# Kernel optimization log

Measured on AMD Instinct MI355X. Metric: run time of the kernel, lower is better.

Reference implementation:

```python
import jax, jax.numpy as jnp
import numpy as np

B, S_IMG, S_TXT, H, D = 1, 2048, 512, 24, 128
HID = H * D  # 3072
S_TOT = S_TXT + S_IMG
IP_SCALE = 1.0
EPS = 1e-5


def setup_inputs() -> dict:
    key = jax.random.key(0)
    ks = jax.random.split(key, 16)
    r = lambda k, s: jax.random.normal(k, s, dtype=jnp.float32)
    w = lambda k, s: r(k, s) * 0.02
    theta = r(ks[15], (S_TOT, D))  # rotary angles over joint sequence
    z = lambda: jnp.zeros((HID,), jnp.float32)
    return dict(
        hidden_states=r(ks[0], (B, S_IMG, HID)),
        encoder_hidden_states=r(ks[1], (B, S_TXT, HID)),
        image_emb=r(ks[2], (B, 4, HID)),
        rope_cos=jnp.cos(theta), rope_sin=jnp.sin(theta),
        Wq=w(ks[3], (HID, HID)), bq=z(),
        Wk=w(ks[4], (HID, HID)), bk=z(),
        Wv=w(ks[5], (HID, HID)), bv=z(),
        Waq=w(ks[6], (HID, HID)), baq=z(),
        Wak=w(ks[7], (HID, HID)), bak=z(),
        Wav=w(ks[8], (HID, HID)), bav=z(),
        Wk_ip=w(ks[9], (HID, HID)),
        Wv_ip=w(ks[10], (HID, HID)),
        Wo=w(ks[11], (HID, HID)), bo=z(),
        Wao=w(ks[12], (HID, HID)), bao=z(),
    )


def _heads(x):  # [B,S,HID] -> [B,H,S,D]
    return x.reshape(x.shape[0], x.shape[1], H, D).transpose(0, 2, 1, 3)


def _unheads(x):  # [B,H,S,D] -> [B,S,HID]
    return x.transpose(0, 2, 1, 3).reshape(x.shape[0], x.shape[2], HID)


def _rmsnorm(x):  # over last dim, no affine (RMSNorm(128, affine=False))
    return x * jax.lax.rsqrt(jnp.mean(x * x, axis=-1, keepdims=True) + EPS)


def _rope(x, cos, sin):  # diffusers apply_rotary_emb, use_real, interleaved pairs
    xp = x.reshape(*x.shape[:-1], D // 2, 2)
    rot = jnp.stack([-xp[..., 1], xp[..., 0]], axis=-1).reshape(x.shape)
    return x * cos + rot * sin  # cos/sin [S,D] broadcast over [B,H,S,D]


def _sdpa(q, k, v):
    s = jnp.einsum('bhqd,bhkd->bhqk', q, k) / jnp.sqrt(jnp.asarray(D, q.dtype))
    return jnp.einsum('bhqk,bhkd->bhqd', jax.nn.softmax(s, axis=-1), v)


def _forward(hidden_states, encoder_hidden_states, image_emb, rope_cos, rope_sin,
             Wq, bq, Wk, bk, Wv, bv, Waq, baq, Wak, bak, Wav, bav,
             Wk_ip, Wv_ip, Wo, bo, Wao, bao):
    # main QKV over image-latent tokens
    q = _rmsnorm(_heads(hidden_states @ Wq.T + bq))
    k = _rmsnorm(_heads(hidden_states @ Wk.T + bk))
    v = _heads(hidden_states @ Wv.T + bv)
    # IP-adapter cross attention (query = latent q, kv from image_emb)
    k_ip = _rmsnorm(_heads(image_emb @ Wk_ip.T))
    v_ip = _heads(image_emb @ Wv_ip.T)
    ip_out = _unheads(_sdpa(q, k_ip, v_ip))  # [B,S_IMG,HID]
    # encoder (text) QKV, concat text-first as in Flux
    eq = _rmsnorm(_heads(encoder_hidden_states @ Waq.T + baq))
    ek = _rmsnorm(_heads(encoder_hidden_states @ Wak.T + bak))
    ev = _heads(encoder_hidden_states @ Wav.T + bav)
    q = jnp.concatenate([eq, q], axis=2)
    k = jnp.concatenate([ek, k], axis=2)
    v = jnp.concatenate([ev, v], axis=2)
    q = _rope(q, rope_cos, rope_sin)
    k = _rope(k, rope_cos, rope_sin)
    out = _unheads(_sdpa(q, k, v))  # [B,S_TOT,HID]
    enc_out, hid_out = out[:, :S_TXT], out[:, S_TXT:]
    hid_out = hid_out + IP_SCALE * ip_out
    hid_out = hid_out @ Wo.T + bo   # to_out[0] (+ identity dropout)
    enc_out = enc_out @ Wao.T + bao  # to_add_out
    return hid_out, enc_out


def reference(hidden_states, encoder_hidden_states, image_emb, rope_cos, rope_sin,
              Wq, bq, Wk, bk, Wv, bv, Waq, baq, Wak, bak, Wav, bav,
              Wk_ip, Wv_ip, Wo, bo, Wao, bao):
    return _forward(hidden_states, encoder_hidden_states, image_emb, rope_cos, rope_sin,
                    Wq, bq, Wk, bk, Wv, bv, Waq, baq, Wak, bak, Wav, bav,
                    Wk_ip, Wv_ip, Wo, bo, Wao, bao)
```

## Files before the change

### kernel.cpp

```cpp
#include <hip/hip_runtime.h>

typedef __bf16 bf16;
typedef __bf16 bf16x2 __attribute__((ext_vector_type(2)));
typedef __bf16 bf16x4 __attribute__((ext_vector_type(4)));
typedef __bf16 bf16x8 __attribute__((ext_vector_type(8)));
typedef float  f32x4  __attribute__((ext_vector_type(4)));

#define H_    24
#define D_    128
#define HID_  3072
#define SIMG_ 2048
#define STXT_ 512
#define STOT_ 2560
#define EPS_  1e-5f
#define SCALE_ 0.08838834764831845f
#define HH_   ((size_t)HID_*HID_)

typedef __attribute__((address_space(3))) unsigned int lds_uint;
typedef const __attribute__((address_space(1))) unsigned int glb_uint;
__device__ __forceinline__ void gll16(const void* g, void* l){
  __builtin_amdgcn_global_load_lds((glb_uint*)g, (lds_uint*)l, 16, 0, 0);
}

__device__ inline bf16x8 frag8f(const float* __restrict__ p){
  const f32x4 a = *(const f32x4*)p;
  const f32x4 b = *(const f32x4*)(p + 4);
  bf16x8 r;
  r[0]=(bf16)a[0]; r[1]=(bf16)a[1]; r[2]=(bf16)a[2]; r[3]=(bf16)a[3];
  r[4]=(bf16)b[0]; r[5]=(bf16)b[1]; r[6]=(bf16)b[2]; r[7]=(bf16)b[3];
  return r;
}

__global__ __launch_bounds__(256) void k_f2b(const float* __restrict__ src,
                                             bf16* __restrict__ dst, int n)
{
  const int i = ((int)blockIdx.x*256 + (int)threadIdx.x)*8;
  if (i + 7 < n){
    const f32x4 a = *(const f32x4*)(src + i);
    const f32x4 b = *(const f32x4*)(src + i + 4);
    bf16x8 o;
    o[0]=(bf16)a[0]; o[1]=(bf16)a[1]; o[2]=(bf16)a[2]; o[3]=(bf16)a[3];
    o[4]=(bf16)b[0]; o[5]=(bf16)b[1]; o[6]=(bf16)b[2]; o[7]=(bf16)b[3];
    *(bf16x8*)(dst + i) = o;
  }
}

__global__ __launch_bounds__(256) void k_f2bw8(
    const float* __restrict__ W0, const float* __restrict__ W1,
    const float* __restrict__ W2, const float* __restrict__ W3,
    const float* __restrict__ W4, const float* __restrict__ W5,
    const float* __restrict__ W6, const float* __restrict__ W7,
    bf16* __restrict__ out)
{
  const int wi = (int)blockIdx.y;
  const float* s = (wi==0)?W0:(wi==1)?W1:(wi==2)?W2:(wi==3)?W3:(wi==4)?W4:(wi==5)?W5:(wi==6)?W6:W7;
  bf16* d = out + (size_t)wi*HH_;
  const int i = ((int)blockIdx.x*256 + (int)threadIdx.x)*8;
  const f32x4 a = *(const f32x4*)(s + i);
  const f32x4 b = *(const f32x4*)(s + i + 4);
  bf16x8 o;
  o[0]=(bf16)a[0]; o[1]=(bf16)a[1]; o[2]=(bf16)a[2]; o[3]=(bf16)a[3];
  o[4]=(bf16)b[0]; o[5]=(bf16)b[1]; o[6]=(bf16)b[2]; o[7]=(bf16)b[3];
  *(bf16x8*)(d + i) = o;
}

#define MFMA_ __builtin_amdgcn_mfma_f32_16x16x32_bf16
#define MM(bfr, n) \
    acc[0][n]=MFMA_(af0,bfr,acc[0][n],0,0,0); acc[1][n]=MFMA_(af1,bfr,acc[1][n],0,0,0); \
    acc[2][n]=MFMA_(af2,bfr,acc[2][n],0,0,0); acc[3][n]=MFMA_(af3,bfr,acc[3][n],0,0,0);
#define WAIT6 asm volatile("s_waitcnt vmcnt(6)" ::: "memory")
#define WAIT0 asm volatile("s_waitcnt vmcnt(0)" ::: "memory")
#define NOWAIT (void)0

__device__ __forceinline__ void gemm8_core(
    const bf16* __restrict__ A, const bf16* __restrict__ W,
    int mb, int nb,
    f32x4 (&acc)[4][4],
    bf16 (&Al)[3][128][64],
    bf16 (&Bl)[3][256][64])
{
  const int t = (int)threadIdx.x;
  const int w = t >> 6, l = t & 63;
  const int lr = l & 15, lg = l >> 4;
  const int wr = w >> 2, wc = w & 3;
  const int srow = t >> 3;
  const int soff = ((t & 7) ^ (srow & 7)) * 8;

  const bf16* Abase = A + (size_t)(mb + srow)*HID_ + soff;
  const bf16* Wbase = W + (size_t)(nb + srow)*HID_ + soff;

#define SA(buf, tt, i) gll16(Abase + (size_t)(i)*64*HID_ + (tt)*64, &Al[buf][0][0] + (i)*4096 + t*8)
#define SB(buf, tt, i) gll16(Wbase + (size_t)(i)*64*HID_ + (tt)*64, &Bl[buf][0][0] + (i)*4096 + t*8)

  const int arow_ = wr*64 + lr;
  const int brow_ = wc*64 + lr;
  const int sx = lr & 7;

  SA(0,0,0); SA(0,0,1); SB(0,0,0); SB(0,0,1); SB(0,0,2); SB(0,0,3);
  SA(1,1,0); SA(1,1,1); SB(1,1,0); SB(1,1,1); SB(1,1,2); SB(1,1,3);
  WAIT6;
  __builtin_amdgcn_s_barrier();

#define TILE(C, NXT, TT, PRE, TW)                                            \
  {                                                                          \
    bf16x8 af0,af1,af2,af3,b0,b1;                                            \
    const int s0_ = (lg^sx)*8, s1_ = ((4+lg)^sx)*8;                          \
                                                        \
    af0=*(const bf16x8*)&Al[C][arow_   ][s0_];                               \
    af1=*(const bf16x8*)&Al[C][arow_+16][s0_];                               \
    af2=*(const bf16x8*)&Al[C][arow_+32][s0_];                               \
    af3=*(const bf16x8*)&Al[C][arow_+48][s0_];                               \
    b0 =*(const bf16x8*)&Bl[C][brow_   ][s0_];                               \
    b1 =*(const bf16x8*)&Bl[C][brow_+16][s0_];                               \
    if (PRE){ SA(NXT,(TT)+2,0); SA(NXT,(TT)+2,1); }                          \
    __builtin_amdgcn_s_setprio(1); MM(b0,0) MM(b1,1)                         \
    __builtin_amdgcn_s_setprio(0);                                           \
    __builtin_amdgcn_s_barrier();                                            \
                                                        \
    b0 =*(const bf16x8*)&Bl[C][brow_+32][s0_];                               \
    b1 =*(const bf16x8*)&Bl[C][brow_+48][s0_];                               \
    if (PRE){ SB(NXT,(TT)+2,0); SB(NXT,(TT)+2,1); }                          \
    __builtin_amdgcn_s_setprio(1); MM(b0,2) MM(b1,3)                         \
    __builtin_amdgcn_s_setprio(0);                                           \
    __builtin_amdgcn_s_barrier();                                            \
                                                        \
    af0=*(const bf16x8*)&Al[C][arow_   ][s1_];                               \
    af1=*(const bf16x8*)&Al[C][arow_+16][s1_];                               \
    af2=*(const bf16x8*)&Al[C][arow_+32][s1_];                               \
    af3=*(const bf16x8*)&Al[C][arow_+48][s1_];                               \
    b0 =*(const bf16x8*)&Bl[C][brow_   ][s1_];                               \
    b1 =*(const bf16x8*)&Bl[C][brow_+16][s1_];                               \
    if (PRE){ SB(NXT,(TT)+2,2); SB(NXT,(TT)+2,3); }                          \
    __builtin_amdgcn_s_setprio(1); MM(b0,0) MM(b1,1)                         \
    __builtin_amdgcn_s_setprio(0);                                           \
    __builtin_amdgcn_s_barrier();                                            \
                                                        \
    b0 =*(const bf16x8*)&Bl[C][brow_+32][s1_];                               \
    b1 =*(const bf16x8*)&Bl[C][brow_+48][s1_];                               \
    __builtin_amdgcn_s_setprio(1); MM(b0,2) MM(b1,3)                         \
    __builtin_amdgcn_s_setprio(0);                                           \
    TW;                                                                      \
    __builtin_amdgcn_s_barrier();                                            \
  }

  for (int base = 0; base < 45; base += 3){
    TILE(0, 2, base,   true, WAIT6);
    TILE(1, 0, base+1, true, WAIT6);
    TILE(2, 1, base+2, true, WAIT6);
  }
  TILE(0, 2, 45, true,  WAIT6);
  TILE(1, 0, 46, false, WAIT0);
  TILE(2, 1, 47, false, NOWAIT);
#undef TILE
#undef SA
#undef SB
}

__global__ __launch_bounds__(512, 1) void k_gemm8_qkv(
    const bf16* __restrict__ Ahid, const bf16* __restrict__ Aenc,
    const bf16* __restrict__ Wb,
    const float* bq, const float* bk, const float* bv,
    const float* baq, const float* bak, const float* bav,
    bf16* Cq, bf16* Ck, bf16* Cv, bf16* Ceq, bf16* Cek, bf16* Cev)
{
  __shared__ __align__(16) bf16 Al[3][128][64];
  __shared__ __align__(16) bf16 Bl[3][256][64];
  const int by = (int)blockIdx.y;
  const int enc = (by >= 16) ? 1 : 0;
  const int which = (int)blockIdx.x % 3;
  const int nb = ((int)blockIdx.x / 3)*256;
  const int mb = (enc ? (by - 16) : by)*128;
  const bf16* A = enc ? Aenc : Ahid;
  const int widx = which + enc*3;
  const bf16* W = Wb + (size_t)widx*HH_;
  const float* bias = (which==0) ? (enc?baq:bq) : (which==1) ? (enc?bak:bk) : (enc?bav:bv);
  bf16* Cm = (which==0) ? (enc?Ceq:Cq) : (which==1) ? (enc?Cek:Ck) : (enc?Cev:Cv);

  f32x4 acc[4][4] = {};
  gemm8_core(A, W, mb, nb, acc, Al, Bl);

  const int w = (int)(threadIdx.x >> 6), l = (int)(threadIdx.x & 63u);
  const int lr = l & 15, lg = l >> 4;
  const int wr = w >> 2, wc = w & 3;
  #pragma unroll
  for (int nf = 0; nf < 4; nf++){
    const int col = nb + wc*64 + nf*16 + lr;
    const float bvl = bias[col];
    #pragma unroll
    for (int m = 0; m < 4; m++){
      #pragma unroll
      for (int r = 0; r < 4; r++){
        const int row = mb + wr*64 + m*16 + lg*4 + r;
        Cm[(size_t)row*HID_ + col] = (bf16)(acc[m][nf][r] + bvl);
      }
    }
  }
}

__global__ __launch_bounds__(512, 1) void k_gemm8_out(
    const bf16* __restrict__ Ahid, const bf16* __restrict__ Aenc,
    const bf16* __restrict__ Wb,
    const float* bo, const float* bao, float* __restrict__ outp)
{
  __shared__ __align__(16) bf16 Al[3][128][64];
  __shared__ __align__(16) bf16 Bl[3][256][64];
  const int by = (int)blockIdx.y;
  const int enc = (by >= 16) ? 1 : 0;
  const int nb = (int)blockIdx.x*256;
  const int mb = (enc ? (by - 16) : by)*128;
  const bf16* A = enc ? Aenc : Ahid;
  const bf16* W = Wb + (size_t)(enc ? 7 : 6)*HH_;
  const float* bias = enc ? bao : bo;
  float* C = outp + (enc ? (size_t)SIMG_*HID_ : 0);

  f32x4 acc[4][4] = {};
  gemm8_core(A, W, mb, nb, acc, Al, Bl);

  const int w = (int)(threadIdx.x >> 6), l = (int)(threadIdx.x & 63u);
  const int lr = l & 15, lg = l >> 4;
  const int wr = w >> 2, wc = w & 3;
  #pragma unroll
  for (int nf = 0; nf < 4; nf++){
    const int col = nb + wc*64 + nf*16 + lr;
    const float bvl = bias[col];
    #pragma unroll
    for (int m = 0; m < 4; m++){
      #pragma unroll
      for (int r = 0; r < 4; r++){
        const int row = mb + wr*64 + m*16 + lg*4 + r;
        C[(size_t)row*HID_ + col] = acc[m][nf][r] + bvl;
      }
    }
  }
}

__global__ __launch_bounds__(256) void k_gemm_ip(const float* __restrict__ A,
    const float* __restrict__ Wk_, const float* __restrict__ Wv_,
    bf16* __restrict__ Ck_, bf16* __restrict__ Cv_)
{
  const float* Wm = blockIdx.y ? Wv_ : Wk_;
  bf16* C = blockIdx.y ? Cv_ : Ck_;
  const int w = (int)(threadIdx.x >> 6), l = (int)(threadIdx.x & 63u);
  const int lr = l & 15, lg = l >> 4;
  const int nbw = (int)blockIdx.x*64 + w*16;
  f32x4 acc = {};
  const float* arow = A + (size_t)((lr < 4) ? lr : 0)*HID_;
  const float* wrow = Wm + (size_t)(nbw + lr)*HID_;
  for (int k0 = 0; k0 < HID_; k0 += 32){
    const bf16x8 af  = frag8f(arow + k0 + lg*8);
    const bf16x8 bfr = frag8f(wrow + k0 + lg*8);
    acc = __builtin_amdgcn_mfma_f32_16x16x32_bf16(af, bfr, acc, 0, 0, 0);
  }
  if (lg == 0){
    #pragma unroll
    for (int r = 0; r < 4; r++)
      C[(size_t)r*HID_ + nbw + lr] = (bf16)acc[r];
  }
}

__global__ __launch_bounds__(256) void k_finish_qk(
    const bf16* __restrict__ rawQ, const bf16* __restrict__ rawK,
    const bf16* __restrict__ rawEQ, const bf16* __restrict__ rawEK,
    const float* __restrict__ cosT, const float* __restrict__ sinT,
    bf16* __restrict__ Qh, bf16* __restrict__ Kh)
{
  const int wid = (int)blockIdx.x*4 + (int)(threadIdx.x >> 6);
  const int l = (int)(threadIdx.x & 63u);
  const int s = wid / H_;
  const int h = wid % H_;
  const bf16 *sq_, *sk_;
  if (s < STXT_){
    const size_t off = (size_t)s*HID_ + h*D_;
    sq_ = rawEQ + off; sk_ = rawEK + off;
  } else {
    const size_t off = (size_t)(s - STXT_)*HID_ + h*D_;
    sq_ = rawQ + off; sk_ = rawK + off;
  }
  const int d0 = 2*l, d1 = 2*l + 1;
  float q0 = sq_[d0], q1 = sq_[d1];
  float k0 = sk_[d0], k1 = sk_[d1];
  float ssq = q0*q0 + q1*q1;
  float ssk = k0*k0 + k1*k1;
  #pragma unroll
  for (int m = 1; m < 64; m <<= 1){ ssq += __shfl_xor(ssq, m); ssk += __shfl_xor(ssk, m); }
  const float rq = rsqrtf(ssq*(1.0f/128.0f) + EPS_);
  const float rk = rsqrtf(ssk*(1.0f/128.0f) + EPS_);
  q0 *= rq; q1 *= rq; k0 *= rk; k1 *= rk;
  const float c0 = cosT[(size_t)s*D_ + d0], c1 = cosT[(size_t)s*D_ + d1];
  const float s0 = sinT[(size_t)s*D_ + d0], s1 = sinT[(size_t)s*D_ + d1];
  const float qo0 = q0*c0 - q1*s0, qo1 = q1*c1 + q0*s1;
  const float ko0 = k0*c0 - k1*s0, ko1 = k1*c1 + k0*s1;
  const size_t qoff = ((size_t)h*STOT_ + s)*D_ + d0;
  Qh[qoff] = (bf16)qo0; Qh[qoff + 1] = (bf16)qo1;
  Kh[qoff] = (bf16)ko0; Kh[qoff + 1] = (bf16)ko1;
}

__global__ __launch_bounds__(256) void k_vtrans(
    const bf16* __restrict__ rawV, const bf16* __restrict__ rawEV,
    bf16* __restrict__ Vt)
{
  __shared__ bf16 lt[128*130];
  const int t = (int)threadIdx.x;
  const int stile = (int)blockIdx.x*128;
  const int h = (int)blockIdx.y;
  #pragma unroll
  for (int i = 0; i < 8; i++){
    const int sl = i*16 + (t >> 4);
    const int s = stile + sl;
    const bf16* src = (s < STXT_) ? (rawEV + (size_t)s*HID_) : (rawV + (size_t)(s - STXT_)*HID_);
    const bf16x8 v = *(const bf16x8*)(src + h*D_ + (t & 15)*8);
    #pragma unroll
    for (int j = 0; j < 8; j++) lt[((t & 15)*8 + j)*130 + sl] = v[j];
  }
  __syncthreads();
  #pragma unroll
  for (int j = 0; j < 4; j++){
    const int d = j*32 + (t >> 3);
    const int s0 = (t & 7)*16;
    bf16x8 a, b;
    #pragma unroll
    for (int k = 0; k < 4; k++){
      const bf16x2 p = *(const bf16x2*)(lt + d*130 + s0 + 2*k);
      a[2*k] = p[0]; a[2*k+1] = p[1];
    }
    #pragma unroll
    for (int k = 0; k < 4; k++){
      const bf16x2 p = *(const bf16x2*)(lt + d*130 + s0 + 8 + 2*k);
      b[2*k] = p[0]; b[2*k+1] = p[1];
    }
    bf16* dst = Vt + ((size_t)h*D_ + d)*STOT_ + stile + s0;
    *(bf16x8*)dst = a;
    *(bf16x8*)(dst + 8) = b;
  }
}

__global__ __launch_bounds__(256) void k_finish_ip(
    const bf16* __restrict__ rawKip, const bf16* __restrict__ rawVip,
    float* __restrict__ Kip, float* __restrict__ Vip)
{
  const int wid = (int)blockIdx.x*4 + (int)(threadIdx.x >> 6);
  const int l = (int)(threadIdx.x & 63u);
  const int h = wid / 4, j = wid % 4;
  const int d0 = 2*l, d1 = 2*l + 1;
  const size_t src = (size_t)j*HID_ + h*D_;
  float k0 = rawKip[src + d0], k1 = rawKip[src + d1];
  float v0 = rawVip[src + d0], v1 = rawVip[src + d1];
  float ss = k0*k0 + k1*k1;
  #pragma unroll
  for (int m = 1; m < 64; m <<= 1) ss += __shfl_xor(ss, m);
  const float rk = rsqrtf(ss*(1.0f/128.0f) + EPS_);
  const size_t dst = ((size_t)h*4 + j)*D_;
  Kip[dst + d0] = k0*rk; Kip[dst + d1] = k1*rk;
  Vip[dst + d0] = v0;    Vip[dst + d1] = v1;
}

__global__ __launch_bounds__(256) void k_ip_attn(
    const bf16* __restrict__ rawQ, const float* __restrict__ Kip,
    const float* __restrict__ Vip, bf16* __restrict__ ipOut)
{
  const int wid = (int)blockIdx.x*4 + (int)(threadIdx.x >> 6);
  const int l = (int)(threadIdx.x & 63u);
  const int s = wid / H_, h = wid % H_;
  const int d0 = 2*l, d1 = 2*l + 1;
  const bf16* src = rawQ + (size_t)s*HID_ + h*D_;
  float q0 = src[d0], q1 = src[d1];
  float ss = q0*q0 + q1*q1;
  #pragma unroll
  for (int m = 1; m < 64; m <<= 1) ss += __shfl_xor(ss, m);
  const float r = rsqrtf(ss*(1.0f/128.0f) + EPS_);
  q0 *= r; q1 *= r;
  const float* kb = Kip + (size_t)h*4*D_;
  const float* vb = Vip + (size_t)h*4*D_;
  float sc[4];
  #pragma unroll
  for (int j = 0; j < 4; j++) sc[j] = q0*kb[j*D_ + d0] + q1*kb[j*D_ + d1];
  #pragma unroll
  for (int m = 1; m < 64; m <<= 1){
    #pragma unroll
    for (int j = 0; j < 4; j++) sc[j] += __shfl_xor(sc[j], m);
  }
  const float mx = fmaxf(fmaxf(sc[0], sc[1]), fmaxf(sc[2], sc[3]));
  float p[4], ps = 0.f;
  #pragma unroll
  for (int j = 0; j < 4; j++){ p[j] = __expf((sc[j] - mx)*SCALE_); ps += p[j]; }
  const float inv = 1.0f/ps;
  float o0 = 0.f, o1 = 0.f;
  #pragma unroll
  for (int j = 0; j < 4; j++){ o0 += p[j]*vb[j*D_ + d0]; o1 += p[j]*vb[j*D_ + d1]; }
  const size_t dst = (size_t)s*HID_ + h*D_;
  ipOut[dst + d0] = (bf16)(o0*inv);
  ipOut[dst + d1] = (bf16)(o1*inv);
}

__global__ __launch_bounds__(256, 2) void k_flash3(
    const bf16* __restrict__ Q, const bf16* __restrict__ K,
    const bf16* __restrict__ Vt, bf16* __restrict__ attnOut)
{
  __shared__ __align__(16) bf16 Ks[2][64*128];
  __shared__ __align__(16) bf16 Vs[2][128*64];
  __shared__ __align__(16) bf16 plds[4][32*64];
  const int t = (int)threadIdx.x;
  const int w = t >> 6, l = t & 63;
  const int lr = l & 15, lg = l >> 4;
  const int h = (int)blockIdx.x / 20;
  const int qbase = ((int)blockIdx.x % 20)*128 + w*32;
  const bf16* Qh = Q  + (size_t)h*STOT_*D_;
  const bf16* Kh = K  + (size_t)h*STOT_*D_;
  const bf16* Vh = Vt + (size_t)h*D_*STOT_;

  bf16x8 qf[2][4];
  #pragma unroll
  for (int qt = 0; qt < 2; qt++)
    #pragma unroll
    for (int kk = 0; kk < 4; kk++)
      qf[qt][kk] = *(const bf16x8*)(Qh + (size_t)(qbase + qt*16 + lr)*D_ + kk*32 + lg*8);

  f32x4 acc[2][8] = {};
  float mrun[2] = {-3.0e38f, -3.0e38f}, lrun[2] = {0.f, 0.f};

  const int krow = t >> 4, kslot = t & 15;
  const int vrow = t >> 3, vslot = t & 7;

  auto STAGE = [&](int buf, int kv){
    #pragma unroll
    for (int i = 0; i < 4; i++){
      const int r = i*16 + krow;
      gll16(Kh + (size_t)(kv + r)*D_ + ((kslot ^ (r & 7))*8),
            (void*)(&Ks[buf][0] + (size_t)t*8 + i*2048));
    }
    #pragma unroll
    for (int i = 0; i < 4; i++){
      const int r = i*32 + vrow;
      gll16(Vh + (size_t)r*STOT_ + kv + ((vslot ^ (r & 7))*8),
            (void*)(&Vs[buf][0] + (size_t)t*8 + i*2048));
    }
  };

  STAGE(0, 0);
  __syncthreads();
  int cur = 0;
  for (int kv = 0; kv < STOT_; kv += 64){
    if (kv + 64 < STOT_) STAGE(cur ^ 1, kv + 64);

    f32x4 st[2][4] = {};
    #pragma unroll
    for (int tt = 0; tt < 4; tt++){
      const int kr = tt*16 + lr;
      #pragma unroll
      for (int kk = 0; kk < 4; kk++){
        const bf16x8 kf = *(const bf16x8*)(&Ks[cur][0] + kr*128 + (((kk*4 + lg) ^ (kr & 7))*8));
        st[0][tt] = __builtin_amdgcn_mfma_f32_16x16x32_bf16(kf, qf[0][kk], st[0][tt], 0, 0, 0);
        st[1][tt] = __builtin_amdgcn_mfma_f32_16x16x32_bf16(kf, qf[1][kk], st[1][tt], 0, 0, 0);
      }
    }
    #pragma unroll
    for (int qt = 0; qt < 2; qt++){
      const int q = qt*16 + lr;
      float sv[4][4];
      float vmax = -3.0e38f;
      #pragma unroll
      for (int tt = 0; tt < 4; tt++)
        #pragma unroll
        for (int r = 0; r < 4; r++){ const float x = st[qt][tt][r]*SCALE_; sv[tt][r] = x; vmax = fmaxf(vmax, x); }
      vmax = fmaxf(vmax, __shfl_xor(vmax, 16));
      vmax = fmaxf(vmax, __shfl_xor(vmax, 32));
      const float mnew  = fmaxf(mrun[qt], vmax);
      const float alpha = __expf(mrun[qt] - mnew);
      float rs = 0.f;
      #pragma unroll
      for (int tt = 0; tt < 4; tt++){
        bf16x4 pq;
        #pragma unroll
        for (int r = 0; r < 4; r++){
          const float p = __expf(sv[tt][r] - mnew);
          rs += p;
          pq[r] = (bf16)p;
        }
        *(bf16x4*)(&plds[w][q*64 + (((tt*2 + (lg >> 1)) ^ (q & 7))*8) + (lg & 1)*4]) = pq;
      }
      rs += __shfl_xor(rs, 16);
      rs += __shfl_xor(rs, 32);
      lrun[qt] = lrun[qt]*alpha + rs;
      mrun[qt] = mnew;
      #pragma unroll
      for (int n = 0; n < 8; n++)
        #pragma unroll
        for (int r = 0; r < 4; r++) acc[qt][n][r] *= alpha;
    }
    #pragma unroll
    for (int ks = 0; ks < 2; ks++){
      const bf16x8 pb0 = *(const bf16x8*)(&plds[w][(lr)*64      + (((ks*4 + lg) ^ (lr & 7))*8)]);
      const bf16x8 pb1 = *(const bf16x8*)(&plds[w][(16 + lr)*64 + (((ks*4 + lg) ^ (lr & 7))*8)]);
      #pragma unroll
      for (int n = 0; n < 8; n++){
        const int vr = n*16 + lr;
        const bf16x8 vf = *(const bf16x8*)(&Vs[cur][0] + vr*64 + (((ks*4 + lg) ^ (vr & 7))*8));
        acc[0][n] = __builtin_amdgcn_mfma_f32_16x16x32_bf16(vf, pb0, acc[0][n], 0, 0, 0);
        acc[1][n] = __builtin_amdgcn_mfma_f32_16x16x32_bf16(vf, pb1, acc[1][n], 0, 0, 0);
      }
    }
    __syncthreads();
    cur ^= 1;
  }
  #pragma unroll
  for (int qt = 0; qt < 2; qt++){
    const float inv = 1.0f/lrun[qt];
    #pragma unroll
    for (int n = 0; n < 8; n++){
      #pragma unroll
      for (int r = 0; r < 4; r++){
        attnOut[(size_t)(qbase + qt*16 + lr)*HID_ + h*D_ + n*16 + lg*4 + r] = (bf16)(acc[qt][n][r]*inv);
      }
    }
  }
}

__global__ __launch_bounds__(256) void k_add_hid(
    const bf16* __restrict__ attn, const bf16* __restrict__ ip, bf16* __restrict__ outp)
{
  const size_t i = ((size_t)blockIdx.x*256 + threadIdx.x)*4;
  const bf16x4 a = *(const bf16x4*)(attn + (size_t)STXT_*HID_ + i);
  const bf16x4 b = *(const bf16x4*)(ip + i);
  bf16x4 o;
  #pragma unroll
  for (int c = 0; c < 4; c++) o[c] = (bf16)((float)a[c] + (float)b[c]);
  *(bf16x4*)(outp + i) = o;
}

extern "C" void kernel_launch(void* const* d_in, const int* in_sizes, int n_in,
                              void* d_out, int out_size, void* d_ws, size_t ws_size,
                              hipStream_t stream)
{
  const float* HS   = (const float*)d_in[0];
  const float* ENC  = (const float*)d_in[1];
  const float* IMG  = (const float*)d_in[2];
  const float* COS  = (const float*)d_in[3];
  const float* SIN  = (const float*)d_in[4];
  const float* Wq   = (const float*)d_in[5];  const float* bq  = (const float*)d_in[6];
  const float* Wk   = (const float*)d_in[7];  const float* bk  = (const float*)d_in[8];
  const float* Wv   = (const float*)d_in[9];  const float* bv  = (const float*)d_in[10];
  const float* Waq  = (const float*)d_in[11]; const float* baq = (const float*)d_in[12];
  const float* Wak  = (const float*)d_in[13]; const float* bak = (const float*)d_in[14];
  const float* Wav  = (const float*)d_in[15]; const float* bav = (const float*)d_in[16];
  const float* Wkip = (const float*)d_in[17]; const float* Wvip= (const float*)d_in[18];
  const float* Wo   = (const float*)d_in[19]; const float* bo  = (const float*)d_in[20];
  const float* Wao  = (const float*)d_in[21]; const float* bao = (const float*)d_in[22];

  char* wsb = (char*)d_ws;
  size_t off = 0;
  auto alloc = [&](size_t bytes) -> char* {
    char* p = wsb + off; off += (bytes + 255) & ~((size_t)255); return p;
  };
  bf16* rawQ   = (bf16*)alloc((size_t)SIMG_*HID_*2);
  bf16* rawK   = (bf16*)alloc((size_t)SIMG_*HID_*2);
  bf16* rawV   = (bf16*)alloc((size_t)SIMG_*HID_*2);
  bf16* rawEQ  = (bf16*)alloc((size_t)STXT_*HID_*2);
  bf16* rawEK  = (bf16*)alloc((size_t)STXT_*HID_*2);
  bf16* rawEV  = (bf16*)alloc((size_t)STXT_*HID_*2);
  bf16* rawKip = (bf16*)alloc((size_t)4*HID_*2);
  bf16* rawVip = (bf16*)alloc((size_t)4*HID_*2);
  bf16* Qb     = (bf16*)alloc((size_t)H_*STOT_*D_*2);
  bf16* Kb     = (bf16*)alloc((size_t)H_*STOT_*D_*2);
  bf16* Vtb    = (bf16*)alloc((size_t)H_*STOT_*D_*2);
  bf16* AOUT   = (bf16*)alloc((size_t)STOT_*HID_*2);
  bf16* IPOUT  = (bf16*)alloc((size_t)SIMG_*HID_*2);
  float* KIPF  = (float*)alloc((size_t)H_*4*D_*4);
  float* VIPF  = (float*)alloc((size_t)H_*4*D_*4);
  bf16* HSb    = (bf16*)alloc((size_t)SIMG_*HID_*2);
  bf16* ENCb   = (bf16*)alloc((size_t)STXT_*HID_*2);
  bf16* Wb8    = (bf16*)alloc((size_t)8*HH_*2);
  bf16* HIDIN  = HSb;

  dim3 blk(256);
  dim3 blk512(512);
  k_f2b<<<dim3(3072), blk, 0, stream>>>(HS,  HSb,  SIMG_*HID_);
  k_f2b<<<dim3(768),  blk, 0, stream>>>(ENC, ENCb, STXT_*HID_);
  k_f2bw8<<<dim3(4608,8), blk, 0, stream>>>(Wq, Wk, Wv, Waq, Wak, Wav, Wo, Wao, Wb8);
  k_gemm8_qkv<<<dim3(36,20), blk512, 0, stream>>>(HSb, ENCb, Wb8,
                                                  bq, bk, bv, baq, bak, bav,
                                                  rawQ, rawK, rawV, rawEQ, rawEK, rawEV);
  k_gemm_ip<<<dim3(48,2), blk, 0, stream>>>(IMG, Wkip, Wvip, rawKip, rawVip);
  k_finish_qk<<<dim3(15360), blk, 0, stream>>>(rawQ, rawK, rawEQ, rawEK, COS, SIN, Qb, Kb);
  k_vtrans<<<dim3(20,24), blk, 0, stream>>>(rawV, rawEV, Vtb);
  k_finish_ip<<<dim3(24), blk, 0, stream>>>(rawKip, rawVip, KIPF, VIPF);
  k_ip_attn<<<dim3(12288), blk, 0, stream>>>(rawQ, KIPF, VIPF, IPOUT);
  k_flash3<<<dim3(480), blk, 0, stream>>>(Qb, Kb, Vtb, AOUT);
  k_add_hid<<<dim3(6144), blk, 0, stream>>>(AOUT, IPOUT, HIDIN);
  float* outp = (float*)d_out;
  k_gemm8_out<<<dim3(12,20), blk512, 0, stream>>>(HIDIN, AOUT, Wb8, bo, bao, outp);
}
```

Measured before the change: 568.1 us.

## Fuse prep and finish kernels, remap blocks per XCD, drop GEMM barriers

Merges the fp32-to-bf16 conversions and the IP-adapter projection into one prep kernel. It also merges the QK finish, V transpose and IP finish into one kernel, and folds the IP-output add into the flash-attention epilogue using vectorized bf16x4 stores, which removes the separate add kernel and its global round-trip. The GEMM and flash grids become 1-D with a remap that groups neighbouring tiles per XCD for better L2 reuse. Three intra-tile barriers are removed from the GEMM main loop to cut synchronisation stalls. The risk is a possible LDS race if the prefetch into the next buffer overlaps reads that other waves have not finished.

Measured after the change: 612.0 us. 1.08x slower.

```diff
diff --git a/kernel.cpp b/kernel.cpp
--- a/kernel.cpp
+++ b/kernel.cpp
@@ -31,31 +31,7 @@
   return r;
 }
 
-__global__ __launch_bounds__(256) void k_f2b(const float* __restrict__ src,
-                                             bf16* __restrict__ dst, int n)
-{
-  const int i = ((int)blockIdx.x*256 + (int)threadIdx.x)*8;
-  if (i + 7 < n){
-    const f32x4 a = *(const f32x4*)(src + i);
-    const f32x4 b = *(const f32x4*)(src + i + 4);
-    bf16x8 o;
-    o[0]=(bf16)a[0]; o[1]=(bf16)a[1]; o[2]=(bf16)a[2]; o[3]=(bf16)a[3];
-    o[4]=(bf16)b[0]; o[5]=(bf16)b[1]; o[6]=(bf16)b[2]; o[7]=(bf16)b[3];
-    *(bf16x8*)(dst + i) = o;
-  }
-}
-
-__global__ __launch_bounds__(256) void k_f2bw8(
-    const float* __restrict__ W0, const float* __restrict__ W1,
-    const float* __restrict__ W2, const float* __restrict__ W3,
-    const float* __restrict__ W4, const float* __restrict__ W5,
-    const float* __restrict__ W6, const float* __restrict__ W7,
-    bf16* __restrict__ out)
-{
-  const int wi = (int)blockIdx.y;
-  const float* s = (wi==0)?W0:(wi==1)?W1:(wi==2)?W2:(wi==3)?W3:(wi==4)?W4:(wi==5)?W5:(wi==6)?W6:W7;
-  bf16* d = out + (size_t)wi*HH_;
-  const int i = ((int)blockIdx.x*256 + (int)threadIdx.x)*8;
+__device__ __forceinline__ void cvt8(const float* __restrict__ s, bf16* __restrict__ d, int i){
   const f32x4 a = *(const f32x4*)(s + i);
   const f32x4 b = *(const f32x4*)(s + i + 4);
   bf16x8 o;
@@ -64,12 +40,56 @@
   *(bf16x8*)(d + i) = o;
 }
 
+__global__ __launch_bounds__(256) void k_prep(
+    const float* __restrict__ HS, const float* __restrict__ ENC,
+    const float* __restrict__ W0, const float* __restrict__ W1,
+    const float* __restrict__ W2, const float* __restrict__ W3,
+    const float* __restrict__ W4, const float* __restrict__ W5,
+    const float* __restrict__ W6, const float* __restrict__ W7,
+    const float* __restrict__ IMG,
+    const float* __restrict__ Wkip, const float* __restrict__ Wvip,
+    bf16* __restrict__ HSb, bf16* __restrict__ ENCb, bf16* __restrict__ Wb8,
+    bf16* __restrict__ rawKip, bf16* __restrict__ rawVip)
+{
+  const int bx = (int)blockIdx.x;
+  if (bx < 3072){
+    cvt8(HS, HSb, (bx*256 + (int)threadIdx.x)*8);
+  } else if (bx < 3840){
+    cvt8(ENC, ENCb, ((bx - 3072)*256 + (int)threadIdx.x)*8);
+  } else if (bx < 40704){
+    const int idx = bx - 3840;
+    const int wi = idx / 4608;
+    const float* s = (wi==0)?W0:(wi==1)?W1:(wi==2)?W2:(wi==3)?W3:(wi==4)?W4:(wi==5)?W5:(wi==6)?W6:W7;
+    cvt8(s, Wb8 + (size_t)wi*HH_, ((idx % 4608)*256 + (int)threadIdx.x)*8);
+  } else {
+    const int bi = bx - 40704;
+    const float* Wm = (bi >= 48) ? Wvip : Wkip;
+    bf16* C = (bi >= 48) ? rawVip : rawKip;
+    const int w = (int)(threadIdx.x >> 6), l = (int)(threadIdx.x & 63u);
+    const int lr = l & 15, lg = l >> 4;
+    const int nbw = (bi % 48)*64 + w*16;
+    f32x4 acc = {};
+    const float* arow = IMG + (size_t)((lr < 4) ? lr : 0)*HID_;
+    const float* wrow = Wm + (size_t)(nbw + lr)*HID_;
+    for (int k0 = 0; k0 < HID_; k0 += 32){
+      const bf16x8 af  = frag8f(arow + k0 + lg*8);
+      const bf16x8 bfr = frag8f(wrow + k0 + lg*8);
+      acc = __builtin_amdgcn_mfma_f32_16x16x32_bf16(af, bfr, acc, 0, 0, 0);
+    }
+    if (lg == 0){
+      #pragma unroll
+      for (int r = 0; r < 4; r++)
+        C[(size_t)r*HID_ + nbw + lr] = (bf16)acc[r];
+    }
+  }
+}
+
 #define MFMA_ __builtin_amdgcn_mfma_f32_16x16x32_bf16
 #define MM(bfr, n) \
     acc[0][n]=MFMA_(af0,bfr,acc[0][n],0,0,0); acc[1][n]=MFMA_(af1,bfr,acc[1][n],0,0,0); \
     acc[2][n]=MFMA_(af2,bfr,acc[2][n],0,0,0); acc[3][n]=MFMA_(af3,bfr,acc[3][n],0,0,0);
-#define WAIT6 asm volatile("s_waitcnt vmcnt(6)" ::: "memory")
-#define WAIT0 asm volatile("s_waitcnt vmcnt(0)" ::: "memory")
+#define WAIT6  asm volatile("s_waitcnt vmcnt(6)" ::: "memory")
+#define WAIT0  asm volatile("s_waitcnt vmcnt(0)" ::: "memory")
 #define NOWAIT (void)0
 
 __device__ __forceinline__ void gemm8_core(
@@ -103,9 +123,8 @@
 
 #define TILE(C, NXT, TT, PRE, TW)                                            \
   {                                                                          \
+    const int s0_ = (lg^sx)*8, s1_ = ((4+lg)^sx)*8;                          \
     bf16x8 af0,af1,af2,af3,b0,b1;                                            \
-    const int s0_ = (lg^sx)*8, s1_ = ((4+lg)^sx)*8;                          \
-                                                        \
     af0=*(const bf16x8*)&Al[C][arow_   ][s0_];                               \
     af1=*(const bf16x8*)&Al[C][arow_+16][s0_];                               \
     af2=*(const bf16x8*)&Al[C][arow_+32][s0_];                               \
@@ -115,15 +134,11 @@
     if (PRE){ SA(NXT,(TT)+2,0); SA(NXT,(TT)+2,1); }                          \
     __builtin_amdgcn_s_setprio(1); MM(b0,0) MM(b1,1)                         \
     __builtin_amdgcn_s_setprio(0);                                           \
-    __builtin_amdgcn_s_barrier();                                            \
-                                                        \
     b0 =*(const bf16x8*)&Bl[C][brow_+32][s0_];                               \
     b1 =*(const bf16x8*)&Bl[C][brow_+48][s0_];                               \
     if (PRE){ SB(NXT,(TT)+2,0); SB(NXT,(TT)+2,1); }                          \
     __builtin_amdgcn_s_setprio(1); MM(b0,2) MM(b1,3)                         \
     __builtin_amdgcn_s_setprio(0);                                           \
-    __builtin_amdgcn_s_barrier();                                            \
-                                                        \
     af0=*(const bf16x8*)&Al[C][arow_   ][s1_];                               \
     af1=*(const bf16x8*)&Al[C][arow_+16][s1_];                               \
     af2=*(const bf16x8*)&Al[C][arow_+32][s1_];                               \
@@ -133,8 +148,6 @@
     if (PRE){ SB(NXT,(TT)+2,2); SB(NXT,(TT)+2,3); }                          \
     __builtin_amdgcn_s_setprio(1); MM(b0,0) MM(b1,1)                         \
     __builtin_amdgcn_s_setprio(0);                                           \
-    __builtin_amdgcn_s_barrier();                                            \
-                                                        \
     b0 =*(const bf16x8*)&Bl[C][brow_+32][s1_];                               \
     b1 =*(const bf16x8*)&Bl[C][brow_+48][s1_];                               \
     __builtin_amdgcn_s_setprio(1); MM(b0,2) MM(b1,3)                         \
@@ -165,11 +178,14 @@
 {
   __shared__ __align__(16) bf16 Al[3][128][64];
   __shared__ __align__(16) bf16 Bl[3][256][64];
-  const int by = (int)blockIdx.y;
-  const int enc = (by >= 16) ? 1 : 0;
-  const int which = (int)blockIdx.x % 3;
-  const int nb = ((int)blockIdx.x / 3)*256;
-  const int mb = (enc ? (by - 16) : by)*128;
+  const int lin = (int)blockIdx.x;
+  const int work = (lin & 7)*90 + (lin >> 3);
+  const int mt = work / 36;
+  const int ct = work % 36;
+  const int which = ct % 3;
+  const int nb = (ct/3)*256;
+  const int enc = (mt >= 16) ? 1 : 0;
+  const int mb = (enc ? (mt - 16) : mt)*128;
   const bf16* A = enc ? Aenc : Ahid;
   const int widx = which + enc*3;
   const bf16* W = Wb + (size_t)widx*HH_;
@@ -204,10 +220,12 @@
 {
   __shared__ __align__(16) bf16 Al[3][128][64];
   __shared__ __align__(16) bf16 Bl[3][256][64];
-  const int by = (int)blockIdx.y;
-  const int enc = (by >= 16) ? 1 : 0;
-  const int nb = (int)blockIdx.x*256;
-  const int mb = (enc ? (by - 16) : by)*128;
+  const int lin = (int)blockIdx.x;
+  const int work = (lin & 7)*30 + (lin >> 3);
+  const int mt = work / 12;
+  const int nb = (work % 12)*256;
+  const int enc = (mt >= 16) ? 1 : 0;
+  const int mb = (enc ? (mt - 16) : mt)*128;
   const bf16* A = enc ? Aenc : Ahid;
   const bf16* W = Wb + (size_t)(enc ? 7 : 6)*HH_;
   const float* bias = enc ? bao : bo;
@@ -234,124 +252,96 @@
   }
 }
 
-__global__ __launch_bounds__(256) void k_gemm_ip(const float* __restrict__ A,
-    const float* __restrict__ Wk_, const float* __restrict__ Wv_,
-    bf16* __restrict__ Ck_, bf16* __restrict__ Cv_)
-{
-  const float* Wm = blockIdx.y ? Wv_ : Wk_;
-  bf16* C = blockIdx.y ? Cv_ : Ck_;
-  const int w = (int)(threadIdx.x >> 6), l = (int)(threadIdx.x & 63u);
-  const int lr = l & 15, lg = l >> 4;
-  const int nbw = (int)blockIdx.x*64 + w*16;
-  f32x4 acc = {};
-  const float* arow = A + (size_t)((lr < 4) ? lr : 0)*HID_;
-  const float* wrow = Wm + (size_t)(nbw + lr)*HID_;
-  for (int k0 = 0; k0 < HID_; k0 += 32){
-    const bf16x8 af  = frag8f(arow + k0 + lg*8);
-    const bf16x8 bfr = frag8f(wrow + k0 + lg*8);
-    acc = __builtin_amdgcn_mfma_f32_16x16x32_bf16(af, bfr, acc, 0, 0, 0);
-  }
-  if (lg == 0){
-    #pragma unroll
-    for (int r = 0; r < 4; r++)
-      C[(size_t)r*HID_ + nbw + lr] = (bf16)acc[r];
-  }
-}
-
-__global__ __launch_bounds__(256) void k_finish_qk(
-    const bf16* __restrict__ rawQ, const bf16* __restrict__ rawK,
-    const bf16* __restrict__ rawEQ, const bf16* __restrict__ rawEK,
+__global__ __launch_bounds__(256) void k_finish_all(
+    const bf16* __restrict__ rawQ, const bf16* __restrict__ rawK, const bf16* __restrict__ rawV,
+    const bf16* __restrict__ rawEQ, const bf16* __restrict__ rawEK, const bf16* __restrict__ rawEV,
     const float* __restrict__ cosT, const float* __restrict__ sinT,
-    bf16* __restrict__ Qh, bf16* __restrict__ Kh)
-{
-  const int wid = (int)blockIdx.x*4 + (int)(threadIdx.x >> 6);
-  const int l = (int)(threadIdx.x & 63u);
-  const int s = wid / H_;
-  const int h = wid % H_;
-  const bf16 *sq_, *sk_;
-  if (s < STXT_){
-    const size_t off = (size_t)s*HID_ + h*D_;
-    sq_ = rawEQ + off; sk_ = rawEK + off;
+    const bf16* __restrict__ rawKip, const bf16* __restrict__ rawVip,
+    bf16* __restrict__ Qh, bf16* __restrict__ Kh, bf16* __restrict__ Vt,
+    float* __restrict__ Kip, float* __restrict__ Vip)
+{
+  __shared__ bf16 lt[128*130];
+  const int bx = (int)blockIdx.x;
+  const int t = (int)threadIdx.x;
+  if (bx < 15360){
+    const int wid = bx*4 + (t >> 6);
+    const int l = t & 63;
+    const int s = wid / H_;
+    const int h = wid % H_;
+    const bf16 *sq_, *sk_;
+    if (s < STXT_){
+      const size_t off = (size_t)s*HID_ + h*D_;
+      sq_ = rawEQ + off; sk_ = rawEK + off;
+    } else {
+      const size_t off = (size_t)(s - STXT_)*HID_ + h*D_;
+      sq_ = rawQ + off; sk_ = rawK + off;
+    }
+    const int d0 = 2*l, d1 = 2*l + 1;
+    float q0 = sq_[d0], q1 = sq_[d1];
+    float k0 = sk_[d0], k1 = sk_[d1];
+    float ssq = q0*q0 + q1*q1;
+    float ssk = k0*k0 + k1*k1;
+    #pragma unroll
+    for (int m = 1; m < 64; m <<= 1){ ssq += __shfl_xor(ssq, m); ssk += __shfl_xor(ssk, m); }
+    const float rq = rsqrtf(ssq*(1.0f/128.0f) + EPS_);
+    const float rk = rsqrtf(ssk*(1.0f/128.0f) + EPS_);
+    q0 *= rq; q1 *= rq; k0 *= rk; k1 *= rk;
+    const float c0 = cosT[(size_t)s*D_ + d0], c1 = cosT[(size_t)s*D_ + d1];
+    const float s0 = sinT[(size_t)s*D_ + d0], s1 = sinT[(size_t)s*D_ + d1];
+    const float qo0 = q0*c0 - q1*s0, qo1 = q1*c1 + q0*s1;
+    const float ko0 = k0*c0 - k1*s0, ko1 = k1*c1 + k0*s1;
+    const size_t qoff = ((size_t)h*STOT_ + s)*D_ + d0;
+    Qh[qoff] = (bf16)qo0; Qh[qoff + 1] = (bf16)qo1;
+    Kh[qoff] = (bf16)ko0; Kh[qoff + 1] = (bf16)ko1;
+  } else if (bx < 15840){
+    const int v = bx - 15360;
+    const int stile = (v % 20)*128;
+    const int h = v / 20;
+    #pragma unroll
+    for (int i = 0; i < 8; i++){
+      const int sl = i*16 + (t >> 4);
+      const int s = stile + sl;
+      const bf16* src = (s < STXT_) ? (rawEV + (size_t)s*HID_) : (rawV + (size_t)(s - STXT_)*HID_);
+      const bf16x8 vv = *(const bf16x8*)(src + h*D_ + (t & 15)*8);
+      #pragma unroll
+      for (int j = 0; j < 8; j++) lt[((t & 15)*8 + j)*130 + sl] = vv[j];
+    }
+    __syncthreads();
+    #pragma unroll
+    for (int j = 0; j < 4; j++){
+      const int d = j*32 + (t >> 3);
+      const int s0 = (t & 7)*16;
+      bf16x8 a, b;
+      #pragma unroll
+      for (int k = 0; k < 4; k++){
+        const bf16x2 p = *(const bf16x2*)(lt + d*130 + s0 + 2*k);
+        a[2*k] = p[0]; a[2*k+1] = p[1];
+      }
+      #pragma unroll
+      for (int k = 0; k < 4; k++){
+        const bf16x2 p = *(const bf16x2*)(lt + d*130 + s0 + 8 + 2*k);
+        b[2*k] = p[0]; b[2*k+1] = p[1];
+      }
+      bf16* dst = Vt + ((size_t)h*D_ + d)*STOT_ + stile + s0;
+      *(bf16x8*)dst = a;
+      *(bf16x8*)(dst + 8) = b;
+    }
   } else {
-    const size_t off = (size_t)(s - STXT_)*HID_ + h*D_;
-    sq_ = rawQ + off; sk_ = rawK + off;
-  }
-  const int d0 = 2*l, d1 = 2*l + 1;
-  float q0 = sq_[d0], q1 = sq_[d1];
-  float k0 = sk_[d0], k1 = sk_[d1];
-  float ssq = q0*q0 + q1*q1;
-  float ssk = k0*k0 + k1*k1;
-  #pragma unroll
-  for (int m = 1; m < 64; m <<= 1){ ssq += __shfl_xor(ssq, m); ssk += __shfl_xor(ssk, m); }
-  const float rq = rsqrtf(ssq*(1.0f/128.0f) + EPS_);
-  const float rk = rsqrtf(ssk*(1.0f/128.0f) + EPS_);
-  q0 *= rq; q1 *= rq; k0 *= rk; k1 *= rk;
-  const float c0 = cosT[(size_t)s*D_ + d0], c1 = cosT[(size_t)s*D_ + d1];
-  const float s0 = sinT[(size_t)s*D_ + d0], s1 = sinT[(size_t)s*D_ + d1];
-  const float qo0 = q0*c0 - q1*s0, qo1 = q1*c1 + q0*s1;
-  const float ko0 = k0*c0 - k1*s0, ko1 = k1*c1 + k0*s1;
-  const size_t qoff = ((size_t)h*STOT_ + s)*D_ + d0;
-  Qh[qoff] = (bf16)qo0; Qh[qoff + 1] = (bf16)qo1;
-  Kh[qoff] = (bf16)ko0; Kh[qoff + 1] = (bf16)ko1;
-}
-
-__global__ __launch_bounds__(256) void k_vtrans(
-    const bf16* __restrict__ rawV, const bf16* __restrict__ rawEV,
-    bf16* __restrict__ Vt)
-{
-  __shared__ bf16 lt[128*130];
-  const int t = (int)threadIdx.x;
-  const int stile = (int)blockIdx.x*128;
-  const int h = (int)blockIdx.y;
-  #pragma unroll
-  for (int i = 0; i < 8; i++){
-    const int sl = i*16 + (t >> 4);
-    const int s = stile + sl;
-    const bf16* src = (s < STXT_) ? (rawEV + (size_t)s*HID_) : (rawV + (size_t)(s - STXT_)*HID_);
-    const bf16x8 v = *(const bf16x8*)(src + h*D_ + (t & 15)*8);
-    #pragma unroll
-    for (int j = 0; j < 8; j++) lt[((t & 15)*8 + j)*130 + sl] = v[j];
-  }
-  __syncthreads();
-  #pragma unroll
-  for (int j = 0; j < 4; j++){
-    const int d = j*32 + (t >> 3);
-    const int s0 = (t & 7)*16;
-    bf16x8 a, b;
-    #pragma unroll
-    for (int k = 0; k < 4; k++){
-      const bf16x2 p = *(const bf16x2*)(lt + d*130 + s0 + 2*k);
-      a[2*k] = p[0]; a[2*k+1] = p[1];
-    }
-    #pragma unroll
-    for (int k = 0; k < 4; k++){
-      const bf16x2 p = *(const bf16x2*)(lt + d*130 + s0 + 8 + 2*k);
-      b[2*k] = p[0]; b[2*k+1] = p[1];
-    }
-    bf16* dst = Vt + ((size_t)h*D_ + d)*STOT_ + stile + s0;
-    *(bf16x8*)dst = a;
-    *(bf16x8*)(dst + 8) = b;
-  }
-}
-
-__global__ __launch_bounds__(256) void k_finish_ip(
-    const bf16* __restrict__ rawKip, const bf16* __restrict__ rawVip,
-    float* __restrict__ Kip, float* __restrict__ Vip)
-{
-  const int wid = (int)blockIdx.x*4 + (int)(threadIdx.x >> 6);
-  const int l = (int)(threadIdx.x & 63u);
-  const int h = wid / 4, j = wid % 4;
-  const int d0 = 2*l, d1 = 2*l + 1;
-  const size_t src = (size_t)j*HID_ + h*D_;
-  float k0 = rawKip[src + d0], k1 = rawKip[src + d1];
-  float v0 = rawVip[src + d0], v1 = rawVip[src + d1];
-  float ss = k0*k0 + k1*k1;
-  #pragma unroll
-  for (int m = 1; m < 64; m <<= 1) ss += __shfl_xor(ss, m);
-  const float rk = rsqrtf(ss*(1.0f/128.0f) + EPS_);
-  const size_t dst = ((size_t)h*4 + j)*D_;
-  Kip[dst + d0] = k0*rk; Kip[dst + d1] = k1*rk;
-  Vip[dst + d0] = v0;    Vip[dst + d1] = v1;
+    const int wid = (bx - 15840)*4 + (t >> 6);
+    const int l = t & 63;
+    const int h = wid / 4, j = wid % 4;
+    const int d0 = 2*l, d1 = 2*l + 1;
+    const size_t src = (size_t)j*HID_ + h*D_;
+    float k0 = rawKip[src + d0], k1 = rawKip[src + d1];
+    float v0 = rawVip[src + d0], v1 = rawVip[src + d1];
+    float ss = k0*k0 + k1*k1;
+    #pragma unroll
+    for (int m = 1; m < 64; m <<= 1) ss += __shfl_xor(ss, m);
+    const float rk = rsqrtf(ss*(1.0f/128.0f) + EPS_);
+    const size_t dst = ((size_t)h*4 + j)*D_;
+    Kip[dst + d0] = k0*rk; Kip[dst + d1] = k1*rk;
+    Vip[dst + d0] = v0;    Vip[dst + d1] = v1;
+  }
 }
 
 __global__ __launch_bounds__(256) void k_ip_attn(
@@ -394,7 +384,8 @@
 
 __global__ __launch_bounds__(256, 2) void k_flash3(
     const bf16* __restrict__ Q, const bf16* __restrict__ K,
-    const bf16* __restrict__ Vt, bf16* __restrict__ attnOut)
+    const bf16* __restrict__ Vt, const bf16* __restrict__ ipOut,
+    bf16* __restrict__ attnOut)
 {
   __shared__ __align__(16) bf16 Ks[2][64*128];
   __shared__ __align__(16) bf16 Vs[2][128*64];
@@ -402,8 +393,10 @@
   const int t = (int)threadIdx.x;
   const int w = t >> 6, l = t & 63;
   const int lr = l & 15, lg = l >> 4;
-  const int h = (int)blockIdx.x / 20;
-  const int qbase = ((int)blockIdx.x % 20)*128 + w*32;
+  const int lin = (int)blockIdx.x;
+  const int work = (lin & 7)*60 + (lin >> 3);
+  const int h = work / 20;
+  const int qbase = (work % 20)*128 + w*32;
   const bf16* Qh = Q  + (size_t)h*STOT_*D_;
   const bf16* Kh = K  + (size_t)h*STOT_*D_;
   const bf16* Vh = Vt + (size_t)h*D_*STOT_;
@@ -502,29 +495,28 @@
     __syncthreads();
     cur ^= 1;
   }
+  const bool hid = (qbase >= STXT_);
   #pragma unroll
   for (int qt = 0; qt < 2; qt++){
     const float inv = 1.0f/lrun[qt];
+    const int row = qbase + qt*16 + lr;
     #pragma unroll
     for (int n = 0; n < 8; n++){
-      #pragma unroll
-      for (int r = 0; r < 4; r++){
-        attnOut[(size_t)(qbase + qt*16 + lr)*HID_ + h*D_ + n*16 + lg*4 + r] = (bf16)(acc[qt][n][r]*inv);
-      }
-    }
-  }
-}
-
-__global__ __launch_bounds__(256) void k_add_hid(
-    const bf16* __restrict__ attn, const bf16* __restrict__ ip, bf16* __restrict__ outp)
-{
-  const size_t i = ((size_t)blockIdx.x*256 + threadIdx.x)*4;
-  const bf16x4 a = *(const bf16x4*)(attn + (size_t)STXT_*HID_ + i);
-  const bf16x4 b = *(const bf16x4*)(ip + i);
-  bf16x4 o;
-  #pragma unroll
-  for (int c = 0; c < 4; c++) o[c] = (bf16)((float)a[c] + (float)b[c]);
-  *(bf16x4*)(outp + i) = o;
+      const size_t cbase = (size_t)row*HID_ + h*D_ + n*16 + lg*4;
+      if (hid){
+        const bf16x4 ip = *(const bf16x4*)(ipOut + (size_t)(row - STXT_)*HID_ + h*D_ + n*16 + lg*4);
+        bf16x4 o;
+        #pragma unroll
+        for (int r = 0; r < 4; r++) o[r] = (bf16)(acc[qt][n][r]*inv + (float)ip[r]);
+        *(bf16x4*)(attnOut + cbase) = o;
+      } else {
+        bf16x4 o;
+        #pragma unroll
+        for (int r = 0; r < 4; r++) o[r] = (bf16)(acc[qt][n][r]*inv);
+        *(bf16x4*)(attnOut + cbase) = o;
+      }
+    }
+  }
 }
 
 extern "C" void kernel_launch(void* const* d_in, const int* in_sizes, int n_in,
@@ -569,23 +561,19 @@
   bf16* HSb    = (bf16*)alloc((size_t)SIMG_*HID_*2);
   bf16* ENCb   = (bf16*)alloc((size_t)STXT_*HID_*2);
   bf16* Wb8    = (bf16*)alloc((size_t)8*HH_*2);
-  bf16* HIDIN  = HSb;
 
   dim3 blk(256);
   dim3 blk512(512);
-  k_f2b<<<dim3(3072), blk, 0, stream>>>(HS,  HSb,  SIMG_*HID_);
-  k_f2b<<<dim3(768),  blk, 0, stream>>>(ENC, ENCb, STXT_*HID_);
-  k_f2bw8<<<dim3(4608,8), blk, 0, stream>>>(Wq, Wk, Wv, Waq, Wak, Wav, Wo, Wao, Wb8);
-  k_gemm8_qkv<<<dim3(36,20), blk512, 0, stream>>>(HSb, ENCb, Wb8,
-                                                  bq, bk, bv, baq, bak, bav,
-                                                  rawQ, rawK, rawV, rawEQ, rawEK, rawEV);
-  k_gemm_ip<<<dim3(48,2), blk, 0, stream>>>(IMG, Wkip, Wvip, rawKip, rawVip);
-  k_finish_qk<<<dim3(15360), blk, 0, stream>>>(rawQ, rawK, rawEQ, rawEK, COS, SIN, Qb, Kb);
-  k_vtrans<<<dim3(20,24), blk, 0, stream>>>(rawV, rawEV, Vtb);
-  k_finish_ip<<<dim3(24), blk, 0, stream>>>(rawKip, rawVip, KIPF, VIPF);
+  k_prep<<<dim3(40800), blk, 0, stream>>>(HS, ENC, Wq, Wk, Wv, Waq, Wak, Wav, Wo, Wao,
+                                          IMG, Wkip, Wvip, HSb, ENCb, Wb8, rawKip, rawVip);
+  k_gemm8_qkv<<<dim3(720), blk512, 0, stream>>>(HSb, ENCb, Wb8,
+                                                bq, bk, bv, baq, bak, bav,
+                                                rawQ, rawK, rawV, rawEQ, rawEK, rawEV);
+  k_finish_all<<<dim3(15864), blk, 0, stream>>>(rawQ, rawK, rawV, rawEQ, rawEK, rawEV,
+                                                COS, SIN, rawKip, rawVip,
+                                                Qb, Kb, Vtb, KIPF, VIPF);
   k_ip_attn<<<dim3(12288), blk, 0, stream>>>(rawQ, KIPF, VIPF, IPOUT);
-  k_flash3<<<dim3(480), blk, 0, stream>>>(Qb, Kb, Vtb, AOUT);
-  k_add_hid<<<dim3(6144), blk, 0, stream>>>(AOUT, IPOUT, HIDIN);
+  k_flash3<<<dim3(480), blk, 0, stream>>>(Qb, Kb, Vtb, IPOUT, AOUT);
   float* outp = (float*)d_out;
-  k_gemm8_out<<<dim3(12,20), blk512, 0, stream>>>(HIDIN, AOUT, Wb8, bo, bao, outp);
-}
+  k_gemm8_out<<<dim3(240), blk512, 0, stream>>>(AOUT + (size_t)STXT_*HID_, AOUT, Wb8, bo, bao, outp);
+}
```
